# Kernel optimization log

Hardware: AMD Instinct MI355X
Metric: run time of the kernel (lower is better)

The kernel has to match this reference:

```python
import jax, jax.numpy as jnp
import numpy as np

ALPHA = 0.2  # LeakyReLU negative slope
NEG_FILL = -9e15


def setup_inputs() -> dict:
    key = jax.random.key(0)
    k_adj, k_x, k_W, k_a = jax.random.split(key, 4)
    n, in_feats, out_feats = 12288, 256, 64
    adj = jax.random.randint(k_adj, (n, n), 0, 2, dtype=jnp.int32)
    x = jax.random.normal(k_x, (n, in_feats), dtype=jnp.float32)
    W = jax.random.normal(k_W, (in_feats, out_feats), dtype=jnp.float32) * 0.1
    a = jax.random.normal(k_a, (2 * out_feats, 1), dtype=jnp.float32) * 0.1
    return {"adj": adj, "x": x, "W": W, "a": a}


def reference(adj, x, W, a):
    out_feats = W.shape[1]
    h = x @ W                                  # (n, out_feats)
    wh1 = h @ a[:out_feats]                    # (n, 1)
    wh2 = h @ a[out_feats:]                    # (n, 1)
    e = jax.nn.leaky_relu(wh1 + wh2, ALPHA)    # (n, 1) -- faithful to source (no transpose)
    # broadcast (n,1) scores against (n,n) adjacency mask
    attention = jnp.where(adj > 0, e, NEG_FILL)
    attention = jax.nn.softmax(attention, axis=1)
    # dropout p=0.0 -> identity (eval mode)
    h_prime = attention @ h                    # (n, out_feats)
    return jax.nn.elu(h_prime)                 # concat=True
```

## Files before the change

### kernel.cpp

```cpp
#include <hip/hip_runtime.h>

#define N_NODES 12288
#define IN_F    256
#define OUT_F   64
#define KSPLIT  4
#define MT      64
#define KC      (N_NODES / KSPLIT)
#define BK      128
#define STEPS   (KC / BK)
#define AST     144

typedef __attribute__((ext_vector_type(8))) short bf16x8;
typedef __attribute__((ext_vector_type(4))) float f32x4;

__device__ __forceinline__ unsigned short f2bf(float f) {
    union { float f; unsigned int i; } v; v.f = f;
    unsigned int x = v.i;
    unsigned int r = x + 0x7FFFu + ((x >> 16) & 1u);
    return (unsigned short)(r >> 16);
}

__global__ __launch_bounds__(256) void k_hT(const float* __restrict__ x,
                                            const float* __restrict__ W,
                                            unsigned short* __restrict__ hT) {
    __shared__ unsigned short WT[OUT_F][IN_F + 8];
    int tid = threadIdx.x;
    for (int idx = tid; idx < IN_F * OUT_F; idx += 256) {
        int k = idx >> 6, n = idx & 63;
        WT[n][k] = f2bf(W[idx]);
    }
    __syncthreads();

    int lane = tid & 63, wave = tid >> 6;
    int q = lane >> 4, ml = lane & 15;
    int i0 = blockIdx.x * MT;
    int row = i0 + 16 * wave + ml;
    const float* xr = x + (size_t)row * IN_F + 8 * q;

    f32x4 acc[4];
    #pragma unroll
    for (int nt = 0; nt < 4; ++nt) acc[nt] = (f32x4){0.f, 0.f, 0.f, 0.f};

    #pragma unroll
    for (int kk = 0; kk < IN_F; kk += 32) {
        float4 x0 = *(const float4*)(xr + kk);
        float4 x1 = *(const float4*)(xr + kk + 4);
        union { bf16x8 v; unsigned short u[8]; } A;
        A.u[0] = f2bf(x0.x); A.u[1] = f2bf(x0.y); A.u[2] = f2bf(x0.z); A.u[3] = f2bf(x0.w);
        A.u[4] = f2bf(x1.x); A.u[5] = f2bf(x1.y); A.u[6] = f2bf(x1.z); A.u[7] = f2bf(x1.w);
        #pragma unroll
        for (int nt = 0; nt < 4; ++nt) {
            bf16x8 bv = *(const bf16x8*)&WT[16 * nt + ml][kk + 8 * q];
            acc[nt] = __builtin_amdgcn_mfma_f32_16x16x32_bf16(A.v, bv, acc[nt], 0, 0, 0);
        }
    }

    #pragma unroll
    for (int nt = 0; nt < 4; ++nt) {
        ushort4 o;
        o.x = f2bf(acc[nt][0]); o.y = f2bf(acc[nt][1]);
        o.z = f2bf(acc[nt][2]); o.w = f2bf(acc[nt][3]);
        *(ushort4*)&hT[(size_t)(16 * nt + ml) * N_NODES + i0 + 16 * wave + 4 * q] = o;
    }
}

__global__ __launch_bounds__(256) void k_spmm(const int* __restrict__ adj,
                                              const unsigned short* __restrict__ hT,
                                              float* __restrict__ s_part,
                                              float* __restrict__ deg_part) {
    __shared__ __align__(16) unsigned short As[2][4][16][AST];

    const int tid  = threadIdx.x;
    const int lane = tid & 63;
    const int wave = tid >> 6;
    const int q    = lane >> 4;
    const int ml   = lane & 15;
    const int i0   = blockIdx.x * MT;
    const int ks   = blockIdx.y;
    const int k0   = ks * KC;

    const int* arow = adj + (size_t)(i0 + 16 * wave) * N_NODES + k0 + 2 * lane;
    const unsigned short* bp = hT + (size_t)ml * N_NODES + k0 + 8 * q;

    union { bf16x8 v; unsigned short u[8]; } ones;
    #pragma unroll
    for (int i = 0; i < 8; ++i) ones.u[i] = 0x3F80;

    f32x4 acc[4], accd;
    #pragma unroll
    for (int nt = 0; nt < 4; ++nt) acc[nt] = (f32x4){0.f, 0.f, 0.f, 0.f};
    accd = (f32x4){0.f, 0.f, 0.f, 0.f};

    int2 st[16];

#define STAGE_ISSUE(sidx) do {                                                 \
    const int* ap_ = arow + (size_t)(sidx) * BK;                               \
    _Pragma("unroll")                                                          \
    for (int rr = 0; rr < 16; ++rr)                                            \
        st[rr] = *(const int2*)(ap_ + (size_t)rr * N_NODES);                   \
} while (0)

#define STAGE_WRITE(b) do {                                                    \
    _Pragma("unroll")                                                          \
    for (int rr = 0; rr < 16; ++rr) {                                          \
        unsigned int t = ((unsigned int)st[rr].x +                             \
                          ((unsigned int)st[rr].y << 16)) * 0x3F80u;           \
        *(unsigned int*)&As[b][wave][rr][2 * lane] = t;                        \
    }                                                                          \
} while (0)

#define BLOAD(koff, B0, B1, B2, B3) do {                                       \
    const unsigned short* bq = bp + (koff);                                    \
    B0 = *(const uint4*)(bq);                                                  \
    B1 = *(const uint4*)(bq + (size_t)16 * N_NODES);                           \
    B2 = *(const uint4*)(bq + (size_t)32 * N_NODES);                           \
    B3 = *(const uint4*)(bq + (size_t)48 * N_NODES);                           \
} while (0)

#define COMP(j, b, B0, B1, B2, B3) do {                                        \
    bf16x8 av = *(const bf16x8*)&As[b][wave][ml][32 * (j) + 8 * q];            \
    acc[0] = __builtin_amdgcn_mfma_f32_16x16x32_bf16(av, *(const bf16x8*)&B0, acc[0], 0, 0, 0); \
    acc[1] = __builtin_amdgcn_mfma_f32_16x16x32_bf16(av, *(const bf16x8*)&B1, acc[1], 0, 0, 0); \
    acc[2] = __builtin_amdgcn_mfma_f32_16x16x32_bf16(av, *(const bf16x8*)&B2, acc[2], 0, 0, 0); \
    acc[3] = __builtin_amdgcn_mfma_f32_16x16x32_bf16(av, *(const bf16x8*)&B3, acc[3], 0, 0, 0); \
    accd   = __builtin_amdgcn_mfma_f32_16x16x32_bf16(av, ones.v,               accd,   0, 0, 0); \
} while (0)

    uint4 b0A, b1A, b2A, b3A;
    uint4 b0B, b1B, b2B, b3B;

    STAGE_ISSUE(0);
    STAGE_WRITE(0);
    BLOAD(0, b0A, b1A, b2A, b3A);

    for (int s = 0; s < STEPS; ++s) {
        const int b  = s & 1;
        const int s1 = (s + 1 < STEPS) ? s + 1 : 0;

        STAGE_ISSUE(s1);

        BLOAD(BK * s + 32, b0B, b1B, b2B, b3B);
        COMP(0, b, b0A, b1A, b2A, b3A);
        BLOAD(BK * s + 64, b0A, b1A, b2A, b3A);
        COMP(1, b, b0B, b1B, b2B, b3B);
        BLOAD(BK * s + 96, b0B, b1B, b2B, b3B);
        COMP(2, b, b0A, b1A, b2A, b3A);
        BLOAD(BK * s1,     b0A, b1A, b2A, b3A);
        COMP(3, b, b0B, b1B, b2B, b3B);

        STAGE_WRITE(b ^ 1);
    }

#undef STAGE_ISSUE
#undef STAGE_WRITE
#undef BLOAD
#undef COMP

    float* sp = s_part + (size_t)ks * ((size_t)N_NODES * OUT_F);
    #pragma unroll
    for (int nt = 0; nt < 4; ++nt) {
        #pragma unroll
        for (int rr = 0; rr < 4; ++rr) {
            int orow = i0 + 16 * wave + 4 * q + rr;
            int ocol = 16 * nt + ml;
            sp[(size_t)orow * OUT_F + ocol] = acc[nt][rr];
        }
    }

    if (ml == 0) {
        #pragma unroll
        for (int rr = 0; rr < 4; ++rr)
            deg_part[ks * N_NODES + i0 + 16 * wave + 4 * q + rr] = accd[rr];
    }
}

__global__ __launch_bounds__(256) void k_out(const float* __restrict__ s_part,
                                             const float* __restrict__ deg_part,
                                             float* __restrict__ out) {
    int idx = blockIdx.x * 256 + threadIdx.x;
    int i = idx >> 6;
    float s = 0.f, deg = 0.f;
    #pragma unroll
    for (int p = 0; p < KSPLIT; ++p) {
        s   += s_part[(size_t)p * ((size_t)N_NODES * OUT_F) + idx];
        deg += deg_part[p * N_NODES + i];
    }
    float v = (deg > 0.5f) ? (s / deg) : 0.f;
    out[idx] = (v > 0.f) ? v : expm1f(v);
}

extern "C" void kernel_launch(void* const* d_in, const int* in_sizes, int n_in,
                              void* d_out, int out_size, void* d_ws, size_t ws_size,
                              hipStream_t stream) {
    const int*   adj = (const int*)d_in[0];
    const float* x   = (const float*)d_in[1];
    const float* W   = (const float*)d_in[2];
    float* out = (float*)d_out;

    char* ws = (char*)d_ws;
    const size_t hT_bytes = (size_t)N_NODES * OUT_F * 2;
    const size_t sp_bytes = (size_t)KSPLIT * N_NODES * OUT_F * 4;
    unsigned short* hT = (unsigned short*)ws;
    float* s_part      = (float*)(ws + hT_bytes);
    float* deg_part    = (float*)(ws + hT_bytes + sp_bytes);

    k_hT  <<<dim3(N_NODES / MT),          dim3(256), 0, stream>>>(x, W, hT);
    k_spmm<<<dim3(N_NODES / MT, KSPLIT),  dim3(256), 0, stream>>>(adj, hT, s_part, deg_part);
    k_out <<<dim3(N_NODES * OUT_F / 256), dim3(256), 0, stream>>>(s_part, deg_part, out);
}
```

Before: 851.9 us.

## Pack adjacency to bytes and load it directly into MFMA operands

Adds a pre-pass that compresses the int32 adjacency into uint8 and rewrites the aggregation kernel to read the packed bytes directly per lane, expanding them to bf16 in registers instead of staging through shared memory. The split-K factor is raised to 8 to create more blocks. This trades an extra full pass over the int32 matrix plus a byte write for a smaller, simpler main loop without LDS traffic or barriers.

```diff
diff --git a/kernel.cpp b/kernel.cpp
--- a/kernel.cpp
+++ b/kernel.cpp
@@ -3,12 +3,10 @@
 #define N_NODES 12288
 #define IN_F    256
 #define OUT_F   64
-#define KSPLIT  4
+#define KSPLIT  8
 #define MT      64
 #define KC      (N_NODES / KSPLIT)
-#define BK      128
-#define STEPS   (KC / BK)
-#define AST     144
+#define STEPS   (KC / 32)
 
 typedef __attribute__((ext_vector_type(8))) short bf16x8;
 typedef __attribute__((ext_vector_type(4))) float f32x4;
@@ -18,6 +16,19 @@
     unsigned int x = v.i;
     unsigned int r = x + 0x7FFFu + ((x >> 16) & 1u);
     return (unsigned short)(r >> 16);
+}
+
+__global__ __launch_bounds__(256) void k_pack(const int* __restrict__ adj,
+                                              unsigned int* __restrict__ adj8) {
+    const size_t total  = (size_t)N_NODES * N_NODES / 4;
+    const size_t stride = (size_t)2048 * 256;
+    size_t i = (size_t)blockIdx.x * 256 + threadIdx.x;
+    #pragma unroll 2
+    for (; i < total; i += stride) {
+        int4 a = ((const int4*)adj)[i];
+        adj8[i] = (unsigned)a.x | ((unsigned)a.y << 8) |
+                  ((unsigned)a.z << 16) | ((unsigned)a.w << 24);
+    }
 }
 
 __global__ __launch_bounds__(256) void k_hT(const float* __restrict__ x,
@@ -64,12 +75,10 @@
     }
 }
 
-__global__ __launch_bounds__(256) void k_spmm(const int* __restrict__ adj,
+__global__ __launch_bounds__(256) void k_spmm(const unsigned char* __restrict__ adj8,
                                               const unsigned short* __restrict__ hT,
                                               float* __restrict__ s_part,
                                               float* __restrict__ deg_part) {
-    __shared__ __align__(16) unsigned short As[2][4][16][AST];
-
     const int tid  = threadIdx.x;
     const int lane = tid & 63;
     const int wave = tid >> 6;
@@ -78,8 +87,9 @@
     const int i0   = blockIdx.x * MT;
     const int ks   = blockIdx.y;
     const int k0   = ks * KC;
+    const int row  = i0 + 16 * wave + ml;
 
-    const int* arow = adj + (size_t)(i0 + 16 * wave) * N_NODES + k0 + 2 * lane;
+    const unsigned char*  ap = adj8 + (size_t)row * N_NODES + k0 + 8 * q;
     const unsigned short* bp = hT + (size_t)ml * N_NODES + k0 + 8 * q;
 
     union { bf16x8 v; unsigned short u[8]; } ones;
@@ -91,69 +101,45 @@
     for (int nt = 0; nt < 4; ++nt) acc[nt] = (f32x4){0.f, 0.f, 0.f, 0.f};
     accd = (f32x4){0.f, 0.f, 0.f, 0.f};
 
-    int2 st[16];
-
-#define STAGE_ISSUE(sidx) do {                                                 \
-    const int* ap_ = arow + (size_t)(sidx) * BK;                               \
-    _Pragma("unroll")                                                          \
-    for (int rr = 0; rr < 16; ++rr)                                            \
-        st[rr] = *(const int2*)(ap_ + (size_t)rr * N_NODES);                   \
-} while (0)
-
-#define STAGE_WRITE(b) do {                                                    \
-    _Pragma("unroll")                                                          \
-    for (int rr = 0; rr < 16; ++rr) {                                          \
-        unsigned int t = ((unsigned int)st[rr].x +                             \
-                          ((unsigned int)st[rr].y << 16)) * 0x3F80u;           \
-        *(unsigned int*)&As[b][wave][rr][2 * lane] = t;                        \
-    }                                                                          \
-} while (0)
-
-#define BLOAD(koff, B0, B1, B2, B3) do {                                       \
-    const unsigned short* bq = bp + (koff);                                    \
+#define LOADS(s, AA, B0, B1, B2, B3) do {                                      \
+    AA = *(const uint2*)(ap + 32 * (size_t)(s));                               \
+    const unsigned short* bq = bp + 32 * (s);                                  \
     B0 = *(const uint4*)(bq);                                                  \
     B1 = *(const uint4*)(bq + (size_t)16 * N_NODES);                           \
     B2 = *(const uint4*)(bq + (size_t)32 * N_NODES);                           \
     B3 = *(const uint4*)(bq + (size_t)48 * N_NODES);                           \
 } while (0)
 
-#define COMP(j, b, B0, B1, B2, B3) do {                                        \
-    bf16x8 av = *(const bf16x8*)&As[b][wave][ml][32 * (j) + 8 * q];            \
-    acc[0] = __builtin_amdgcn_mfma_f32_16x16x32_bf16(av, *(const bf16x8*)&B0, acc[0], 0, 0, 0); \
-    acc[1] = __builtin_amdgcn_mfma_f32_16x16x32_bf16(av, *(const bf16x8*)&B1, acc[1], 0, 0, 0); \
-    acc[2] = __builtin_amdgcn_mfma_f32_16x16x32_bf16(av, *(const bf16x8*)&B2, acc[2], 0, 0, 0); \
-    acc[3] = __builtin_amdgcn_mfma_f32_16x16x32_bf16(av, *(const bf16x8*)&B3, acc[3], 0, 0, 0); \
-    accd   = __builtin_amdgcn_mfma_f32_16x16x32_bf16(av, ones.v,               accd,   0, 0, 0); \
+#define COMP(AA, B0, B1, B2, B3) do {                                          \
+    unsigned int u_ = AA.x, v_ = AA.y;                                         \
+    union { bf16x8 v; unsigned int w[4]; } av_;                                \
+    av_.w[0] = ((u_ & 0xFFu)         | ((u_ & 0xFF00u) << 8)) * 0x3F80u;       \
+    av_.w[1] = (((u_ >> 16) & 0xFFu) | ((u_ >> 24) << 16))    * 0x3F80u;       \
+    av_.w[2] = ((v_ & 0xFFu)         | ((v_ & 0xFF00u) << 8)) * 0x3F80u;       \
+    av_.w[3] = (((v_ >> 16) & 0xFFu) | ((v_ >> 24) << 16))    * 0x3F80u;       \
+    acc[0] = __builtin_amdgcn_mfma_f32_16x16x32_bf16(av_.v, *(const bf16x8*)&B0, acc[0], 0, 0, 0); \
+    acc[1] = __builtin_amdgcn_mfma_f32_16x16x32_bf16(av_.v, *(const bf16x8*)&B1, acc[1], 0, 0, 0); \
+    acc[2] = __builtin_amdgcn_mfma_f32_16x16x32_bf16(av_.v, *(const bf16x8*)&B2, acc[2], 0, 0, 0); \
+    acc[3] = __builtin_amdgcn_mfma_f32_16x16x32_bf16(av_.v, *(const bf16x8*)&B3, acc[3], 0, 0, 0); \
+    accd   = __builtin_amdgcn_mfma_f32_16x16x32_bf16(av_.v, ones.v,              accd,   0, 0, 0); \
 } while (0)
 
+    uint2 aA, aB;
     uint4 b0A, b1A, b2A, b3A;
     uint4 b0B, b1B, b2B, b3B;
 
-    STAGE_ISSUE(0);
-    STAGE_WRITE(0);
-    BLOAD(0, b0A, b1A, b2A, b3A);
+    LOADS(0, aA, b0A, b1A, b2A, b3A);
+    for (int s = 0; s < STEPS - 2; s += 2) {
+        LOADS(s + 1, aB, b0B, b1B, b2B, b3B);
+        COMP(aA, b0A, b1A, b2A, b3A);
+        LOADS(s + 2, aA, b0A, b1A, b2A, b3A);
+        COMP(aB, b0B, b1B, b2B, b3B);
+    }
+    LOADS(STEPS - 1, aB, b0B, b1B, b2B, b3B);
+    COMP(aA, b0A, b1A, b2A, b3A);
+    COMP(aB, b0B, b1B, b2B, b3B);
 
-    for (int s = 0; s < STEPS; ++s) {
-        const int b  = s & 1;
-        const int s1 = (s + 1 < STEPS) ? s + 1 : 0;
-
-        STAGE_ISSUE(s1);
-
-        BLOAD(BK * s + 32, b0B, b1B, b2B, b3B);
-        COMP(0, b, b0A, b1A, b2A, b3A);
-        BLOAD(BK * s + 64, b0A, b1A, b2A, b3A);
-        COMP(1, b, b0B, b1B, b2B, b3B);
-        BLOAD(BK * s + 96, b0B, b1B, b2B, b3B);
-        COMP(2, b, b0A, b1A, b2A, b3A);
-        BLOAD(BK * s1,     b0A, b1A, b2A, b3A);
-        COMP(3, b, b0B, b1B, b2B, b3B);
-
-        STAGE_WRITE(b ^ 1);
-    }
-
-#undef STAGE_ISSUE
-#undef STAGE_WRITE
-#undef BLOAD
+#undef LOADS
 #undef COMP
 
     float* sp = s_part + (size_t)ks * ((size_t)N_NODES * OUT_F);
@@ -198,13 +184,16 @@
     float* out = (float*)d_out;
 
     char* ws = (char*)d_ws;
-    const size_t hT_bytes = (size_t)N_NODES * OUT_F * 2;
-    const size_t sp_bytes = (size_t)KSPLIT * N_NODES * OUT_F * 4;
-    unsigned short* hT = (unsigned short*)ws;
-    float* s_part      = (float*)(ws + hT_bytes);
-    float* deg_part    = (float*)(ws + hT_bytes + sp_bytes);
+    const size_t hT_bytes  = (size_t)N_NODES * OUT_F * 2;
+    const size_t sp_bytes  = (size_t)KSPLIT * N_NODES * OUT_F * 4;
+    const size_t dp_bytes  = (size_t)KSPLIT * N_NODES * 4;
+    unsigned short* hT     = (unsigned short*)ws;
+    float* s_part          = (float*)(ws + hT_bytes);
+    float* deg_part        = (float*)(ws + hT_bytes + sp_bytes);
+    unsigned char* adj8    = (unsigned char*)(ws + hT_bytes + sp_bytes + dp_bytes);
 
+    k_pack<<<dim3(2048),                  dim3(256), 0, stream>>>(adj, (unsigned int*)adj8);
     k_hT  <<<dim3(N_NODES / MT),          dim3(256), 0, stream>>>(x, W, hT);
-    k_spmm<<<dim3(N_NODES / MT, KSPLIT),  dim3(256), 0, stream>>>(adj, hT, s_part, deg_part);
+    k_spmm<<<dim3(N_NODES / MT, KSPLIT),  dim3(256), 0, stream>>>(adj8, hT, s_part, deg_part);
     k_out <<<dim3(N_NODES * OUT_F / 256), dim3(256), 0, stream>>>(s_part, deg_part, out);
 }
```

Result: slower. 1.037 ms (+21.7%).
